# Performance work log

Hardware: AMD Instinct MI355X
Metric: run time of the kernel (lower is better)

The kernel has to match this reference:

```python
import jax, jax.numpy as jnp
import numpy as np

CUTOFF = 5.0  # Angstrom, from __init__ default
BOX = 50.0    # box edge length
N = 4096      # number of atoms


def setup_inputs() -> dict:
    key = jax.random.key(0)
    k1, _ = jax.random.split(key)
    # positions uniform in the box [0, BOX)^3
    q = jax.random.uniform(k1, (N, 3), dtype=jnp.float32) * BOX
    cell = jnp.full((3,), BOX, dtype=jnp.float32)
    return {"q": q, "cell": cell}


def reference(q, cell):
    # q: [N, 3] flat coordinates (forward does q.reshape(-1, 3))
    xyz = q.reshape(-1, 3)
    # dis_mat[i, j] = xyz[j] - xyz[i]  (matches xyz[None,:,:] - xyz[:,None,:])
    dis_mat = xyz[None, :, :] - xyz[:, None, :]              # [N, N, 3]
    # minimum-image convention: shift components outside [-cell/2, cell/2)
    offsets = (dis_mat < -0.5 * cell).astype(dis_mat.dtype) \
              - (dis_mat >= 0.5 * cell).astype(dis_mat.dtype)  # [N, N, 3]
    dis_mat = dis_mat + offsets * cell
    dis_sq = jnp.sum(dis_mat * dis_mat, axis=-1)             # [N, N]
    mask = (dis_sq < CUTOFF ** 2) & (dis_sq != 0.0)          # cutoff + exclude self
    # upper-triangular neighbor selection (torch.triu(mask).nonzero());
    # return the triu-masked squared distances (fixed shape, jit-friendly)
    triu_mask = jnp.triu(mask)                               # [N, N] bool
    return jnp.where(triu_mask, dis_sq, 0.0)
```

## Files before the change

kernel.cpp:

```cpp
#include <hip/hip_runtime.h>

#define N_ATOMS 4096
#define CUTOFF_SQ 25.0f

__global__ __launch_bounds__(256) void pairdist_kernel(
    const float* __restrict__ q,
    const float* __restrict__ cell,
    float* __restrict__ out)
{
    const int rowgrp = blockIdx.x >> 2;
    const int i0 = rowgrp << 2;
    const int colt = ((blockIdx.x & 3) << 8) + threadIdx.x;
    const int j0 = colt << 2;

    float* outp = out + (size_t)i0 * N_ATOMS + j0;

    if (j0 < i0) {
        const float4 z = make_float4(0.f, 0.f, 0.f, 0.f);
#pragma unroll
        for (int r = 0; r < 4; ++r)
            *reinterpret_cast<float4*>(outp + (size_t)r * N_ATOMS) = z;
        return;
    }

    const float cx = cell[0], cy = cell[1], cz = cell[2];

    const float* qi = q + 3 * i0;
    float xi[4], yi[4], zi[4];
#pragma unroll
    for (int r = 0; r < 4; ++r) {
        xi[r] = qi[3 * r + 0];
        yi[r] = qi[3 * r + 1];
        zi[r] = qi[3 * r + 2];
    }

    const float4* q4 = reinterpret_cast<const float4*>(q);
    const float4 a = q4[3 * colt + 0];
    const float4 b = q4[3 * colt + 1];
    const float4 c = q4[3 * colt + 2];
    const float xj[4] = {a.x, a.w, b.z, c.y};
    const float yj[4] = {a.y, b.x, b.w, c.z};
    const float zj[4] = {a.z, b.y, c.x, c.w};

#pragma unroll
    for (int r = 0; r < 4; ++r) {
        float res[4];
#pragma unroll
        for (int k = 0; k < 4; ++k) {
            float dx = fabsf(xj[k] - xi[r]); dx = fminf(dx, cx - dx);
            float dy = fabsf(yj[k] - yi[r]); dy = fminf(dy, cy - dy);
            float dz = fabsf(zj[k] - zi[r]); dz = fminf(dz, cz - dz);
            const float d2 = dx * dx + dy * dy + dz * dz;
            const bool keep = (d2 < CUTOFF_SQ) & (d2 != 0.0f) &
                              ((j0 + k) >= (i0 + r));
            res[k] = keep ? d2 : 0.0f;
        }
        *reinterpret_cast<float4*>(outp + (size_t)r * N_ATOMS) =
            make_float4(res[0], res[1], res[2], res[3]);
    }
}

extern "C" void kernel_launch(void* const* d_in, const int* in_sizes, int n_in,
                              void* d_out, int out_size, void* d_ws, size_t ws_size,
                              hipStream_t stream) {
    const float* q    = (const float*)d_in[0];
    const float* cell = (const float*)d_in[1];
    float* out = (float*)d_out;

    const int grid = 4096;
    pairdist_kernel<<<grid, 256, 0, stream>>>(q, cell, out);
}
```

Baseline: 16.30 us.

## Widen per-thread tile to 4x8 and use nontemporal output stores

Each thread now computes 8 columns instead of 4, so the grid is halved and each thread issues two 16-byte stores per row. All output stores, including the zero-fill of the lower triangle, use nontemporal hints to bypass cache retention on the 64 MB write stream. The early-exit test for fully-below-diagonal tiles is adjusted to the wider tile. Fewer threads may reduce the latency hiding available for this store-bound kernel.

```diff
diff --git a/kernel.cpp b/kernel.cpp
--- a/kernel.cpp
+++ b/kernel.cpp
@@ -2,24 +2,29 @@
 
 #define N_ATOMS 4096
 #define CUTOFF_SQ 25.0f
+
+typedef float f4 __attribute__((ext_vector_type(4)));
 
 __global__ __launch_bounds__(256) void pairdist_kernel(
     const float* __restrict__ q,
     const float* __restrict__ cell,
     float* __restrict__ out)
 {
-    const int rowgrp = blockIdx.x >> 2;
+    const int rowgrp = blockIdx.x >> 1;
     const int i0 = rowgrp << 2;
-    const int colt = ((blockIdx.x & 3) << 8) + threadIdx.x;
-    const int j0 = colt << 2;
+    const int colt = ((blockIdx.x & 1) << 8) + threadIdx.x;
+    const int j0 = colt << 3;
 
     float* outp = out + (size_t)i0 * N_ATOMS + j0;
 
-    if (j0 < i0) {
-        const float4 z = make_float4(0.f, 0.f, 0.f, 0.f);
+    if (j0 + 8 <= i0) {
+        const f4 z = {0.f, 0.f, 0.f, 0.f};
 #pragma unroll
-        for (int r = 0; r < 4; ++r)
-            *reinterpret_cast<float4*>(outp + (size_t)r * N_ATOMS) = z;
+        for (int r = 0; r < 4; ++r) {
+            float* rp = outp + (size_t)r * N_ATOMS;
+            __builtin_nontemporal_store(z, reinterpret_cast<f4*>(rp));
+            __builtin_nontemporal_store(z, reinterpret_cast<f4*>(rp + 4));
+        }
         return;
     }
 
@@ -34,29 +39,30 @@
         zi[r] = qi[3 * r + 2];
     }
 
-    const float4* q4 = reinterpret_cast<const float4*>(q);
-    const float4 a = q4[3 * colt + 0];
-    const float4 b = q4[3 * colt + 1];
-    const float4 c = q4[3 * colt + 2];
-    const float xj[4] = {a.x, a.w, b.z, c.y};
-    const float yj[4] = {a.y, b.x, b.w, c.z};
-    const float zj[4] = {a.z, b.y, c.x, c.w};
+    union { f4 v[6]; float s[24]; } u;
+    const f4* q4 = reinterpret_cast<const f4*>(q);
+#pragma unroll
+    for (int m = 0; m < 6; ++m) u.v[m] = q4[6 * colt + m];
 
 #pragma unroll
     for (int r = 0; r < 4; ++r) {
-        float res[4];
+        const float xr = xi[r], yr = yi[r], zr = zi[r];
+        const int ir = i0 + r;
+        float res[8];
 #pragma unroll
-        for (int k = 0; k < 4; ++k) {
-            float dx = fabsf(xj[k] - xi[r]); dx = fminf(dx, cx - dx);
-            float dy = fabsf(yj[k] - yi[r]); dy = fminf(dy, cy - dy);
-            float dz = fabsf(zj[k] - zi[r]); dz = fminf(dz, cz - dz);
-            const float d2 = dx * dx + dy * dy + dz * dz;
-            const bool keep = (d2 < CUTOFF_SQ) & (d2 != 0.0f) &
-                              ((j0 + k) >= (i0 + r));
+        for (int k = 0; k < 8; ++k) {
+            float dx = fabsf(u.s[3 * k + 0] - xr); dx = fminf(dx, cx - dx);
+            float dy = fabsf(u.s[3 * k + 1] - yr); dy = fminf(dy, cy - dy);
+            float dz = fabsf(u.s[3 * k + 2] - zr); dz = fminf(dz, cz - dz);
+            const float d2 = fmaf(dz, dz, fmaf(dy, dy, dx * dx));
+            const bool keep = (d2 < CUTOFF_SQ) & (d2 != 0.0f) & ((j0 + k) >= ir);
             res[k] = keep ? d2 : 0.0f;
         }
-        *reinterpret_cast<float4*>(outp + (size_t)r * N_ATOMS) =
-            make_float4(res[0], res[1], res[2], res[3]);
+        float* rp = outp + (size_t)r * N_ATOMS;
+        f4 lo = {res[0], res[1], res[2], res[3]};
+        f4 hi = {res[4], res[5], res[6], res[7]};
+        __builtin_nontemporal_store(lo, reinterpret_cast<f4*>(rp));
+        __builtin_nontemporal_store(hi, reinterpret_cast<f4*>(rp + 4));
     }
 }
 
@@ -67,6 +73,6 @@
     const float* cell = (const float*)d_in[1];
     float* out = (float*)d_out;
 
-    const int grid = 4096;
+    const int grid = 2048;
     pairdist_kernel<<<grid, 256, 0, stream>>>(q, cell, out);
 }
```

Result: slower. 26.94 us (+65.3%).
